# Performance work log

Hardware: AMD Instinct MI355X
Metric: run time of the kernel (lower is better)

Reference implementation:

```python
import jax, jax.numpy as jnp
import numpy as np

N_NODES = 50000
N_EDGES = 1_600_000
F_IN = 32
HIDDEN = 32
HORIZON = 12
K = 2


def setup_inputs() -> dict:
    key = jax.random.key(0)
    ks = jax.random.split(key, 12)
    s = 0.1  # keep gates away from saturation
    x = jax.random.normal(ks[0], (N_NODES, 1, F_IN), dtype=jnp.float32)
    edge_index = jax.random.randint(ks[1], (2, N_EDGES), 0, N_NODES, dtype=jnp.int64)
    edge_weight = jax.random.uniform(ks[2], (N_EDGES,), dtype=jnp.float32)
    Wx = jax.random.normal(ks[3], (4, K, F_IN, HIDDEN), dtype=jnp.float32) * s
    bx = jax.random.normal(ks[4], (4, HIDDEN), dtype=jnp.float32) * s
    Wh = jax.random.normal(ks[5], (4, K, HIDDEN, HIDDEN), dtype=jnp.float32) * s
    bh = jax.random.normal(ks[6], (4, HIDDEN), dtype=jnp.float32) * s
    wc = jax.random.normal(ks[7], (3, HIDDEN), dtype=jnp.float32) * s
    b = jax.random.normal(ks[8], (4, HIDDEN), dtype=jnp.float32) * s
    W_lin = jax.random.normal(ks[9], (HIDDEN, HORIZON), dtype=jnp.float32) * s
    b_lin = jax.random.normal(ks[10], (HORIZON,), dtype=jnp.float32) * s
    h0 = jnp.zeros((N_NODES, HIDDEN), dtype=jnp.float32)
    c0 = jnp.zeros((N_NODES, HIDDEN), dtype=jnp.float32)
    return dict(x=x, edge_index=edge_index, edge_weight=edge_weight, Wx=Wx, bx=bx,
                Wh=Wh, bh=bh, wc=wc, b=b, W_lin=W_lin, b_lin=b_lin, h0=h0, c0=c0)


def reference(x, edge_index, edge_weight, Wx, bx, Wh, bh, wc, b, W_lin, b_lin, h0, c0):
    N = x.shape[0]
    src, dst = edge_index[0], edge_index[1]
    # ChebConv sym normalization with lambda_max=2: L_hat = L - I = -D^{-1/2} A D^{-1/2}
    deg = jax.ops.segment_sum(edge_weight, src, num_segments=N)
    dinv = jnp.where(deg > 0, jax.lax.rsqrt(deg), 0.0)
    nw = -dinv[src] * edge_weight * dinv[dst]  # [E]

    X = x[:, 0, :]  # squeeze(1) -> [N, F]

    def cheb(Z, W, bb):
        # K=2 Chebyshev: T0(Z)=Z, T1(Z)=L_hat Z (sparse gather-scatter)
        LZ = jax.ops.segment_sum(nw[:, None] * Z[src], dst, num_segments=N)
        return Z @ W[0] + LZ @ W[1] + bb

    # gate order: i, f, c, o
    I = jax.nn.sigmoid(cheb(X, Wx[0], bx[0]) + cheb(h0, Wh[0], bh[0]) + wc[0] * c0 + b[0])
    Fg = jax.nn.sigmoid(cheb(X, Wx[1], bx[1]) + cheb(h0, Wh[1], bh[1]) + wc[1] * c0 + b[1])
    T = jnp.tanh(cheb(X, Wx[2], bx[2]) + cheb(h0, Wh[2], bh[2]) + b[2])
    C = Fg * c0 + I * T
    O = jax.nn.sigmoid(cheb(X, Wx[3], bx[3]) + cheb(h0, Wh[3], bh[3]) + wc[2] * C + b[3])
    H = O * jnp.tanh(C)

    h = jax.nn.relu(H) @ W_lin + b_lin  # Linear(32, horizon)
    return (h, H, C)
```

## Files before the change

kernel.cpp:

```cpp
#include <hip/hip_runtime.h>
#include <math.h>

#define HID 32
#define HOR 12
#define NB  256
#define GSH 8
#define GW  256
#define NPT 4
#define TILE 4096
#define SBINS 256

__device__ __forceinline__ float sigmoidf_(float x) { return 1.0f / (1.0f + expf(-x)); }


__global__ __launch_bounds__(1024) void k_hist(const int* __restrict__ src,
                                               const int* __restrict__ dst,
                                               int* __restrict__ hist,
                                               const float* __restrict__ h0,
                                               const float* __restrict__ c0,
                                               int* __restrict__ flag,
                                               int E, int chunk, int ng, int total4) {
    __shared__ int hS[GW], hD[GW];
    int t = threadIdx.x, b = blockIdx.x;
    for (int i = t; i < ng; i += 1024) { hS[i] = 0; hD[i] = 0; }
    __syncthreads();
    int beg = b * chunk, end = min(E, beg + chunk);
    for (int e = beg + t; e < end; e += 1024) {
        atomicAdd(&hS[src[e] >> GSH], 1);
        atomicAdd(&hD[dst[e] >> GSH], 1);
    }
    bool ah = false, ac = false;
    for (int i = b * 1024 + t; i < total4; i += NB * 1024) {
        float4 a = ((const float4*)h0)[i];
        float4 c = ((const float4*)c0)[i];
        ah |= (a.x != 0.0f) | (a.y != 0.0f) | (a.z != 0.0f) | (a.w != 0.0f);
        ac |= (c.x != 0.0f) | (c.y != 0.0f) | (c.z != 0.0f) | (c.w != 0.0f);
    }
    unsigned long long bh = __ballot(ah);
    unsigned long long bc = __ballot(ac);
    if ((t & 63) == 0) {
        int m = (bh ? 1 : 0) | (bc ? 2 : 0);
        if (m) atomicOr(flag, m);
    }
    __syncthreads();
    for (int i = t; i < ng; i += 1024) {
        hist[(size_t)i * NB + b] = hS[i];
        hist[((size_t)ng + i) * NB + b] = hD[i];
    }
}

__global__ __launch_bounds__(256) void k_binscan(const int* __restrict__ hist,
                                                 int* __restrict__ off,
                                                 int* __restrict__ binTot, int ng2) {
    __shared__ int s[256];
    int b2 = blockIdx.x, t = threadIdx.x;
    int v = hist[(size_t)b2 * NB + t];
    s[t] = v;
    __syncthreads();
    for (int o = 1; o < 256; o <<= 1) {
        int x = (t >= o) ? s[t - o] : 0;
        __syncthreads();
        s[t] += x;
        __syncthreads();
    }
    off[(size_t)t * ng2 + b2] = s[t] - v;
    if (t == 255) binTot[b2] = s[255];
}

__global__ __launch_bounds__(1024) void k_binbase(const int* __restrict__ binTot,
                                                  int* __restrict__ baseS, int* __restrict__ baseD,
                                                  int* __restrict__ rowptr,
                                                  int E, int ng, int N) {
    __shared__ int buf[1024];
    int t = threadIdx.x;
    int isD = blockIdx.x;
    int sum = (t < ng) ? binTot[isD * ng + t] : 0;
    buf[t] = sum;
    __syncthreads();
    for (int o = 1; o < 1024; o <<= 1) {
        int v = (t >= o) ? buf[t - o] : 0;
        __syncthreads();
        buf[t] += v;
        __syncthreads();
    }
    int base = buf[t] - sum;
    int* B = isD ? baseD : baseS;
    if (t < ng) B[t] = base;
    if (t == 0) { B[ng] = E; if (!isD) rowptr[N] = E; }
}

__global__ __launch_bounds__(1024) void k_scatter(const int* __restrict__ src,
                                                  const int* __restrict__ dst,
                                                  const float* __restrict__ w,
                                                  const int* __restrict__ off,
                                                  const int* __restrict__ baseS,
                                                  const int* __restrict__ baseD,
                                                  int2* __restrict__ tmpS, int2* __restrict__ tmpD,
                                                  int E, int chunk, int ng) {
    __shared__ int2 stage[TILE];
    __shared__ int cnt[SBINS];
    __shared__ int gcur[SBINS];
    int t = threadIdx.x, b = blockIdx.x;
    int beg = b * chunk, end = min(E, beg + chunk);
    int ng2 = 2 * ng;

    for (int pass = 0; pass < 2; ++pass) {
        if (t < ng) gcur[t] = (pass == 0) ? off[(size_t)b * ng2 + t] + baseS[t]
                                          : off[(size_t)b * ng2 + ng + t] + baseD[t];
        __syncthreads();

        for (int tb = beg; tb < end; tb += TILE) {
            int tcount = min(TILE, end - tb);
            if (t < SBINS) cnt[t] = 0;
            __syncthreads();

            int g_[4], r_[4];
            int2 p_[4];
            #pragma unroll
            for (int u = 0; u < 4; ++u) {
                int li = u * 1024 + t;
                g_[u] = -1;
                if (li < tcount) {
                    int e = tb + li;
                    int s = src[e];
                    int wb = __float_as_int(w[e]);
                    int g;
                    if (pass == 0) { g = s >> GSH; p_[u] = make_int2(s, wb); }
                    else {
                        int d = dst[e]; g = d >> GSH;
                        p_[u] = make_int2(s | ((d & (GW - 1)) << 16) | (g << 24), wb);
                    }
                    g_[u] = g;
                    r_[u] = atomicAdd(&cnt[g], 1);
                }
            }
            __syncthreads();

            int c = (t < SBINS) ? cnt[t] : 0;
            for (int o = 1; o < SBINS; o <<= 1) {
                int v = (t < SBINS && t >= o) ? cnt[t - o] : 0;
                __syncthreads();
                if (t < SBINS && t >= o) cnt[t] += v;
                __syncthreads();
            }
            if (t < SBINS) cnt[t] -= c;
            __syncthreads();

            #pragma unroll
            for (int u = 0; u < 4; ++u)
                if (g_[u] >= 0) stage[cnt[g_[u]] + r_[u]] = p_[u];
            __syncthreads();

            int2* out = (pass == 0) ? tmpS : tmpD;
            for (int i = t; i < tcount; i += 1024) {
                int2 p = stage[i];
                int g = (pass == 0) ? (p.x >> GSH) : ((p.x >> 24) & 255);
                out[gcur[g] + (i - cnt[g])] = p;
            }
            __syncthreads();

            if (t < SBINS) gcur[t] += c;
            __syncthreads();
        }
        __syncthreads();
    }
}

__global__ __launch_bounds__(1024) void k_degsum(const int2* __restrict__ tmpS,
                                                 const int* __restrict__ baseS,
                                                 float* __restrict__ dinv, int N) {
    __shared__ float h[GW];
    int g = blockIdx.x, t = threadIdx.x;
    if (t < GW) h[t] = 0.0f;
    __syncthreads();
    int beg = baseS[g], end = baseS[g + 1];
    for (int i = beg + t; i < end; i += 1024) {
        int2 p = tmpS[i];
        atomicAdd(&h[p.x & (GW - 1)], __int_as_float(p.y));
    }
    __syncthreads();
    if (t < GW) {
        int n = (g << GSH) + t;
        if (n < N) { float s = h[t]; dinv[n] = (s > 0.0f) ? rsqrtf(s) : 0.0f; }
    }
}

__global__ __launch_bounds__(1024) void k_scatter2(const int2* __restrict__ tmpD,
                                                   const int* __restrict__ baseD,
                                                   const float* __restrict__ dinv,
                                                   int* __restrict__ rowptr,
                                                   int2* __restrict__ epair, int N) {
    __shared__ int h[GW], cur[GW];
    int g = blockIdx.x, t = threadIdx.x;
    if (t < GW) h[t] = 0;
    __syncthreads();
    int beg = baseD[g], end = baseD[g + 1];
    for (int i = beg + t; i < end; i += 1024) atomicAdd(&h[(tmpD[i].x >> 16) & (GW - 1)], 1);
    __syncthreads();
    int v = (t < GW) ? h[t] : 0;
    for (int o = 1; o < GW; o <<= 1) {
        int x = (t < GW && t >= o) ? h[t - o] : 0;
        __syncthreads();
        if (t < GW && t >= o) h[t] += x;
        __syncthreads();
    }
    if (t < GW) {
        int excl = h[t] - v;
        int n = (g << GSH) + t;
        if (n < N) rowptr[n] = beg + excl;
        cur[t] = beg + excl;
    }
    __syncthreads();
    for (int i = beg + t; i < end; i += 1024) {
        int2 p = tmpD[i];
        int low = (p.x >> 16) & (GW - 1);
        int s = p.x & 0xFFFF;
        int pos = atomicAdd(&cur[low], 1);
        float nw = -dinv[s] * __int_as_float(p.y) * dinv[(g << GSH) + low];
        epair[pos] = make_int2(s, __float_as_int(nw));
    }
}

__global__ __launch_bounds__(256) void k_gather(const int* __restrict__ rowptr,
                                                const int2* __restrict__ epair,
                                                const float* __restrict__ X,
                                                const float* __restrict__ H0,
                                                const int* __restrict__ hflag,
                                                float* __restrict__ LX, float* __restrict__ LH,
                                                int N) {
    int tid = blockIdx.x * 256 + threadIdx.x;
    int n = tid >> 5;
    int f = tid & 31;
    if (n >= N) return;
    int beg = rowptr[n], end = rowptr[n + 1];
    float acc = 0.0f, accH = 0.0f;
    int fl = *hflag;
    if (fl & 1) {
        #pragma unroll 4
        for (int i = beg; i < end; ++i) {
            int2 p = epair[i];
            float w = __int_as_float(p.y);
            acc  += w * X[(p.x << 5) + f];
            accH += w * H0[(p.x << 5) + f];
        }
    } else {
        #pragma unroll 4
        for (int i = beg; i < end; ++i) {
            int2 p = epair[i];
            acc += __int_as_float(p.y) * X[(p.x << 5) + f];
        }
    }
    LX[(n << 5) + f] = acc;
    if (fl & 1) LH[(n << 5) + f] = accH;
}

__global__ __launch_bounds__(256) void k_gates(
    const float* __restrict__ X, const float* __restrict__ LX,
    const float* __restrict__ H0, const float* __restrict__ LH,
    const float* __restrict__ C0,
    const float* __restrict__ Wx, const float* __restrict__ bx,
    const float* __restrict__ Wh, const float* __restrict__ bh,
    const float* __restrict__ wc, const float* __restrict__ b,
    const int* __restrict__ flag,
    float* __restrict__ outH, float* __restrict__ outC, int N) {
    int tid = blockIdx.x * 256 + threadIdx.x;
    int g = tid >> 5;
    int j = tid & 31;
    int n0 = g * NPT;
    if (n0 >= N) return;
    int cnt = min(NPT, N - n0);
    int f2 = *flag;

    if (f2 == 0) {
        float xk[NPT], lxk[NPT];
        #pragma unroll
        for (int i = 0; i < NPT; ++i) { xk[i] = 0.0f; lxk[i] = 0.0f; }
        for (int i = 0; i < cnt; ++i) {
            int base = (n0 + i) << 5;
            xk[i]  = X[base + j];
            lxk[i] = LX[base + j];
        }
        float p0[NPT], p2[NPT], p3[NPT];
        float b0 = bx[0 * HID + j] + bh[0 * HID + j] + b[0 * HID + j];
        float b2 = bx[2 * HID + j] + bh[2 * HID + j] + b[2 * HID + j];
        float b3 = bx[3 * HID + j] + bh[3 * HID + j] + b[3 * HID + j];
        #pragma unroll
        for (int i = 0; i < NPT; ++i) { p0[i] = b0; p2[i] = b2; p3[i] = b3; }

        #pragma unroll 4
        for (int k = 0; k < HID; ++k) {
            int row = k * HID + j;
            float w00 = Wx[row],            w01 = Wx[1024 + row];
            float w20 = Wx[2 * 2048 + row], w21 = Wx[2 * 2048 + 1024 + row];
            float w30 = Wx[3 * 2048 + row], w31 = Wx[3 * 2048 + 1024 + row];
            #pragma unroll
            for (int i = 0; i < NPT; ++i) {
                float xv  = __shfl(xk[i],  k, 32);
                float lxv = __shfl(lxk[i], k, 32);
                p0[i] += xv * w00 + lxv * w01;
                p2[i] += xv * w20 + lxv * w21;
                p3[i] += xv * w30 + lxv * w31;
            }
        }

        float wc2 = wc[2 * HID + j];
        for (int i = 0; i < cnt; ++i) {
            int base = (n0 + i) << 5;
            float I = sigmoidf_(p0[i]);
            float T = tanhf(p2[i]);
            float C = I * T;
            float O = sigmoidf_(p3[i] + wc2 * C);
            outH[base + j] = O * tanhf(C);
            outC[base + j] = C;
        }
        return;
    }

    float xk[NPT], lxk[NPT], hk[NPT], lhk[NPT];
    #pragma unroll
    for (int i = 0; i < NPT; ++i) { xk[i] = 0.0f; lxk[i] = 0.0f; hk[i] = 0.0f; lhk[i] = 0.0f; }
    for (int i = 0; i < cnt; ++i) {
        int base = (n0 + i) << 5;
        xk[i]  = X[base + j];
        lxk[i] = LX[base + j];
        hk[i]  = H0[base + j];
        lhk[i] = (f2 & 1) ? LH[base + j] : 0.0f;
    }

    float pre[4][NPT];
    #pragma unroll
    for (int gt = 0; gt < 4; ++gt) {
        float bb = bx[gt * HID + j] + bh[gt * HID + j] + b[gt * HID + j];
        #pragma unroll
        for (int i = 0; i < NPT; ++i) pre[gt][i] = bb;
    }

    #pragma unroll 2
    for (int k = 0; k < HID; ++k) {
        float w0[4], w1[4], w2[4], w3[4];
        int row = k * HID + j;
        #pragma unroll
        for (int gt = 0; gt < 4; ++gt) {
            w0[gt] = Wx[gt * 2048 + row];
            w1[gt] = Wx[gt * 2048 + 1024 + row];
            w2[gt] = Wh[gt * 2048 + row];
            w3[gt] = Wh[gt * 2048 + 1024 + row];
        }
        #pragma unroll
        for (int i = 0; i < NPT; ++i) {
            float xv  = __shfl(xk[i],  k, 32);
            float lxv = __shfl(lxk[i], k, 32);
            float hv  = __shfl(hk[i],  k, 32);
            float lhv = __shfl(lhk[i], k, 32);
            #pragma unroll
            for (int gt = 0; gt < 4; ++gt)
                pre[gt][i] += xv * w0[gt] + lxv * w1[gt] + hv * w2[gt] + lhv * w3[gt];
        }
    }

    float wc0 = wc[0 * HID + j], wc1 = wc[1 * HID + j], wc2 = wc[2 * HID + j];
    for (int i = 0; i < cnt; ++i) {
        int base = (n0 + i) << 5;
        float c0v = C0[base + j];
        float I  = sigmoidf_(pre[0][i] + wc0 * c0v);
        float Fg = sigmoidf_(pre[1][i] + wc1 * c0v);
        float T  = tanhf(pre[2][i]);
        float C  = Fg * c0v + I * T;
        float O  = sigmoidf_(pre[3][i] + wc2 * C);
        float H  = O * tanhf(C);
        outH[base + j] = H;
        outC[base + j] = C;
    }
}

__global__ void k_head(const float* __restrict__ H, const float* __restrict__ Wl,
                       const float* __restrict__ bl, float* __restrict__ hout, int N) {
    int tid = blockIdx.x * 256 + threadIdx.x;
    int n = tid / HOR;
    int t = tid - n * HOR;
    if (n >= N) return;
    float acc = bl[t];
    #pragma unroll
    for (int k = 0; k < HID; ++k) {
        float v = H[(n << 5) + k];
        acc += fmaxf(v, 0.0f) * Wl[k * HOR + t];
    }
    hout[n * HOR + t] = acc;
}

extern "C" void kernel_launch(void* const* d_in, const int* in_sizes, int n_in,
                              void* d_out, int out_size, void* d_ws, size_t ws_size,
                              hipStream_t stream) {
    const float* x  = (const float*)d_in[0];
    const int*   ei = (const int*)d_in[1];
    const float* ew = (const float*)d_in[2];
    const float* Wx = (const float*)d_in[3];
    const float* bx = (const float*)d_in[4];
    const float* Wh = (const float*)d_in[5];
    const float* bh = (const float*)d_in[6];
    const float* wc = (const float*)d_in[7];
    const float* b  = (const float*)d_in[8];
    const float* Wl = (const float*)d_in[9];
    const float* bl = (const float*)d_in[10];
    const float* h0 = (const float*)d_in[11];
    const float* c0 = (const float*)d_in[12];

    int N = in_sizes[0] / HID;
    int E = in_sizes[2];
    const int* src = ei;
    const int* dst = ei + E;

    int ng = (N + GW - 1) >> GSH;
    int ng2 = 2 * ng;
    int chunk = (E + NB - 1) / NB;

    int* wsi = (int*)d_ws;
    int2*  tmpD   = (int2*)wsi;
    int2*  tmpS   = (int2*)(wsi + 2 * (size_t)E);
    int2*  epair  = tmpS;
    float* LX     = (float*)(wsi + 4 * (size_t)E);
    float* LH     = LX + (size_t)N * HID;
    int*   rowptr = (int*)(LH + (size_t)N * HID);
    int*   hist   = rowptr + (N + 1);
    int*   off    = hist + (size_t)ng2 * NB;
    int*   binTot = off + (size_t)ng2 * NB;
    int*   baseS  = binTot + 2048;
    int*   baseD  = baseS + (ng + 1);
    float* dinv   = (float*)(baseD + (ng + 1));
    int*   flag   = (int*)(dinv + N);

    float* hOut = (float*)d_out;
    float* HOut = hOut + (size_t)N * HOR;
    float* COut = HOut + (size_t)N * HID;

    hipMemsetAsync(flag, 0, sizeof(int), stream);

    k_hist<<<NB, 1024, 0, stream>>>(src, dst, hist, h0, c0, flag, E, chunk, ng, (N * HID) >> 2);
    k_binscan<<<ng2, 256, 0, stream>>>(hist, off, binTot, ng2);
    k_binbase<<<2, 1024, 0, stream>>>(binTot, baseS, baseD, rowptr, E, ng, N);
    k_scatter<<<NB, 1024, 0, stream>>>(src, dst, ew, off, baseS, baseD, tmpS, tmpD, E, chunk, ng);
    k_degsum<<<ng, 1024, 0, stream>>>(tmpS, baseS, dinv, N);
    k_scatter2<<<ng, 1024, 0, stream>>>(tmpD, baseD, dinv, rowptr, epair, N);

    k_gather<<<(N * HID + 255) / 256, 256, 0, stream>>>(rowptr, epair, x, h0, flag, LX, LH, N);

    int gThreads = ((N + NPT - 1) / NPT) * 32;
    k_gates<<<(gThreads + 255) / 256, 256, 0, stream>>>(x, LX, h0, LH, c0,
                                                        Wx, bx, Wh, bh, wc, b, flag,
                                                        HOut, COut, N);

    k_head<<<(N * HOR + 255) / 256, 256, 0, stream>>>(HOut, Wl, bl, hOut, N);
}
```

Measured before the change: 241.1 us.

## Fuse bin-base scan into binscan and merge src/dst scatter passes

Removes the separate k_binbase launch: the last k_binscan block, detected through a global atomic counter, computes the src and dst base offsets. k_scatter now does the src and dst partitioning in a single pass over the edges, reading src, dst and weight once and staging both outputs in LDS, with the tile halved to 2048 to fit. This cuts one kernel launch and one full re-read of the edge arrays. The cost is more LDS per block and the assumption that ng is at most 256, since the fused scan only has 256 threads where the old one had 1024.

```diff
diff --git a/kernel.cpp b/kernel.cpp
--- a/kernel.cpp
+++ b/kernel.cpp
@@ -7,7 +7,7 @@
 #define GSH 8
 #define GW  256
 #define NPT 4
-#define TILE 4096
+#define TILE 2048
 #define SBINS 256
 
 __device__ __forceinline__ float sigmoidf_(float x) { return 1.0f / (1.0f + expf(-x)); }
@@ -51,7 +51,11 @@
 
 __global__ __launch_bounds__(256) void k_binscan(const int* __restrict__ hist,
                                                  int* __restrict__ off,
-                                                 int* __restrict__ binTot, int ng2) {
+                                                 int* __restrict__ binTot,
+                                                 int* __restrict__ baseS, int* __restrict__ baseD,
+                                                 int* __restrict__ rowptr,
+                                                 int* __restrict__ counter,
+                                                 int ng2, int ng, int E, int N) {
     __shared__ int s[256];
     int b2 = blockIdx.x, t = threadIdx.x;
     int v = hist[(size_t)b2 * NB + t];
@@ -65,28 +69,30 @@
     }
     off[(size_t)t * ng2 + b2] = s[t] - v;
     if (t == 255) binTot[b2] = s[255];
-}
-
-__global__ __launch_bounds__(1024) void k_binbase(const int* __restrict__ binTot,
-                                                  int* __restrict__ baseS, int* __restrict__ baseD,
-                                                  int* __restrict__ rowptr,
-                                                  int E, int ng, int N) {
-    __shared__ int buf[1024];
-    int t = threadIdx.x;
-    int isD = blockIdx.x;
-    int sum = (t < ng) ? binTot[isD * ng + t] : 0;
-    buf[t] = sum;
-    __syncthreads();
-    for (int o = 1; o < 1024; o <<= 1) {
-        int v = (t >= o) ? buf[t - o] : 0;
-        __syncthreads();
-        buf[t] += v;
-        __syncthreads();
-    }
-    int base = buf[t] - sum;
-    int* B = isD ? baseD : baseS;
-    if (t < ng) B[t] = base;
-    if (t == 0) { B[ng] = E; if (!isD) rowptr[N] = E; }
+
+    __threadfence();
+    __shared__ int lastFlag;
+    if (t == 0) lastFlag = (atomicAdd(counter, 1) == ng2 - 1) ? 1 : 0;
+    __syncthreads();
+    if (!lastFlag) return;
+
+    __shared__ int bufS[256], bufD[256];
+    int vS = 0, vD = 0;
+    if (t < ng) {
+        vS = __hip_atomic_load(&binTot[t], __ATOMIC_RELAXED, __HIP_MEMORY_SCOPE_AGENT);
+        vD = __hip_atomic_load(&binTot[ng + t], __ATOMIC_RELAXED, __HIP_MEMORY_SCOPE_AGENT);
+    }
+    bufS[t] = vS; bufD[t] = vD;
+    __syncthreads();
+    for (int o = 1; o < 256; o <<= 1) {
+        int xS = (t >= o) ? bufS[t - o] : 0;
+        int xD = (t >= o) ? bufD[t - o] : 0;
+        __syncthreads();
+        bufS[t] += xS; bufD[t] += xD;
+        __syncthreads();
+    }
+    if (t < ng) { baseS[t] = bufS[t] - vS; baseD[t] = bufD[t] - vD; }
+    if (t == 0) { baseS[ng] = E; baseD[ng] = E; rowptr[N] = E; }
 }
 
 __global__ __launch_bounds__(1024) void k_scatter(const int* __restrict__ src,
@@ -97,71 +103,80 @@
                                                   const int* __restrict__ baseD,
                                                   int2* __restrict__ tmpS, int2* __restrict__ tmpD,
                                                   int E, int chunk, int ng) {
-    __shared__ int2 stage[TILE];
-    __shared__ int cnt[SBINS];
-    __shared__ int gcur[SBINS];
+    __shared__ int2 stageS[TILE], stageD[TILE];
+    __shared__ int cntS[SBINS], cntD[SBINS];
+    __shared__ int gcS[SBINS], gcD[SBINS];
     int t = threadIdx.x, b = blockIdx.x;
     int beg = b * chunk, end = min(E, beg + chunk);
     int ng2 = 2 * ng;
-
-    for (int pass = 0; pass < 2; ++pass) {
-        if (t < ng) gcur[t] = (pass == 0) ? off[(size_t)b * ng2 + t] + baseS[t]
-                                          : off[(size_t)b * ng2 + ng + t] + baseD[t];
-        __syncthreads();
-
-        for (int tb = beg; tb < end; tb += TILE) {
-            int tcount = min(TILE, end - tb);
-            if (t < SBINS) cnt[t] = 0;
+    if (t < ng) {
+        gcS[t] = off[(size_t)b * ng2 + t] + baseS[t];
+        gcD[t] = off[(size_t)b * ng2 + ng + t] + baseD[t];
+    }
+    __syncthreads();
+
+    for (int tb = beg; tb < end; tb += TILE) {
+        int tcount = min(TILE, end - tb);
+        if (t < SBINS) { cntS[t] = 0; cntD[t] = 0; }
+        __syncthreads();
+
+        int gS_[2], rS_[2], gD_[2], rD_[2];
+        int2 pS_[2], pD_[2];
+        #pragma unroll
+        for (int u = 0; u < 2; ++u) {
+            int li = u * 1024 + t;
+            gS_[u] = -1;
+            if (li < tcount) {
+                int e = tb + li;
+                int s = src[e], d = dst[e];
+                int wb = __float_as_int(w[e]);
+                int gs = s >> GSH, gd = d >> GSH;
+                pS_[u] = make_int2(s, wb);
+                pD_[u] = make_int2(s | ((d & (GW - 1)) << 16) | (gd << 24), wb);
+                gS_[u] = gs; gD_[u] = gd;
+                rS_[u] = atomicAdd(&cntS[gs], 1);
+                rD_[u] = atomicAdd(&cntD[gd], 1);
+            }
+        }
+        __syncthreads();
+
+        int lt = t & 255;
+        bool isS = (t < 256), isD2 = (t >= 256 && t < 512);
+        int origS = isS ? cntS[lt] : 0;
+        int origD = isD2 ? cntD[lt] : 0;
+        for (int o = 1; o < SBINS; o <<= 1) {
+            int vS = (isS && lt >= o) ? cntS[lt - o] : 0;
+            int vD = (isD2 && lt >= o) ? cntD[lt - o] : 0;
             __syncthreads();
-
-            int g_[4], r_[4];
-            int2 p_[4];
-            #pragma unroll
-            for (int u = 0; u < 4; ++u) {
-                int li = u * 1024 + t;
-                g_[u] = -1;
-                if (li < tcount) {
-                    int e = tb + li;
-                    int s = src[e];
-                    int wb = __float_as_int(w[e]);
-                    int g;
-                    if (pass == 0) { g = s >> GSH; p_[u] = make_int2(s, wb); }
-                    else {
-                        int d = dst[e]; g = d >> GSH;
-                        p_[u] = make_int2(s | ((d & (GW - 1)) << 16) | (g << 24), wb);
-                    }
-                    g_[u] = g;
-                    r_[u] = atomicAdd(&cnt[g], 1);
-                }
+            if (isS && lt >= o) cntS[lt] += vS;
+            if (isD2 && lt >= o) cntD[lt] += vD;
+            __syncthreads();
+        }
+        if (isS) cntS[lt] -= origS;
+        if (isD2) cntD[lt] -= origD;
+        __syncthreads();
+
+        #pragma unroll
+        for (int u = 0; u < 2; ++u) {
+            if (gS_[u] >= 0) {
+                stageS[cntS[gS_[u]] + rS_[u]] = pS_[u];
+                stageD[cntD[gD_[u]] + rD_[u]] = pD_[u];
             }
-            __syncthreads();
-
-            int c = (t < SBINS) ? cnt[t] : 0;
-            for (int o = 1; o < SBINS; o <<= 1) {
-                int v = (t < SBINS && t >= o) ? cnt[t - o] : 0;
-                __syncthreads();
-                if (t < SBINS && t >= o) cnt[t] += v;
-                __syncthreads();
-            }
-            if (t < SBINS) cnt[t] -= c;
-            __syncthreads();
-
-            #pragma unroll
-            for (int u = 0; u < 4; ++u)
-                if (g_[u] >= 0) stage[cnt[g_[u]] + r_[u]] = p_[u];
-            __syncthreads();
-
-            int2* out = (pass == 0) ? tmpS : tmpD;
-            for (int i = t; i < tcount; i += 1024) {
-                int2 p = stage[i];
-                int g = (pass == 0) ? (p.x >> GSH) : ((p.x >> 24) & 255);
-                out[gcur[g] + (i - cnt[g])] = p;
-            }
-            __syncthreads();
-
-            if (t < SBINS) gcur[t] += c;
-            __syncthreads();
-        }
+        }
+        __syncthreads();
+
+        for (int i = t; i < tcount; i += 1024) {
+            int2 p = stageS[i];
+            int g = p.x >> GSH;
+            tmpS[gcS[g] + (i - cntS[g])] = p;
+            int2 q = stageD[i];
+            int g2 = (q.x >> 24) & 255;
+            tmpD[gcD[g2] + (i - cntD[g2])] = q;
+        }
+        __syncthreads();
+
+        if (isS) gcS[lt] += origS;
+        if (isD2) gcD[lt] += origD;
         __syncthreads();
     }
 }
@@ -428,16 +443,17 @@
     int*   baseD  = baseS + (ng + 1);
     float* dinv   = (float*)(baseD + (ng + 1));
     int*   flag   = (int*)(dinv + N);
+    int*   counter= flag + 1;
 
     float* hOut = (float*)d_out;
     float* HOut = hOut + (size_t)N * HOR;
     float* COut = HOut + (size_t)N * HID;
 
-    hipMemsetAsync(flag, 0, sizeof(int), stream);
+    hipMemsetAsync(flag, 0, 2 * sizeof(int), stream);
 
     k_hist<<<NB, 1024, 0, stream>>>(src, dst, hist, h0, c0, flag, E, chunk, ng, (N * HID) >> 2);
-    k_binscan<<<ng2, 256, 0, stream>>>(hist, off, binTot, ng2);
-    k_binbase<<<2, 1024, 0, stream>>>(binTot, baseS, baseD, rowptr, E, ng, N);
+    k_binscan<<<ng2, 256, 0, stream>>>(hist, off, binTot, baseS, baseD, rowptr, counter,
+                                       ng2, ng, E, N);
     k_scatter<<<NB, 1024, 0, stream>>>(src, dst, ew, off, baseS, baseD, tmpS, tmpD, E, chunk, ng);
     k_degsum<<<ng, 1024, 0, stream>>>(tmpS, baseS, dinv, N);
     k_scatter2<<<ng, 1024, 0, stream>>>(tmpD, baseD, dinv, rowptr, epair, N);
```

After: 283.5 us. 17.6% more time.
